# Kernel tuning notes

Hardware: AMD Instinct MI355X
Metric: run time of the kernel (lower is better)

The kernel has to match this reference:

```python
import jax, jax.numpy as jnp
import numpy as np

T, B, D = 2048, 8, 1024
TINY = float(np.finfo(np.float32).tiny)


def _uniform(k, shape, fan_in):
    b = 1.0 / np.sqrt(fan_in)
    return jax.random.uniform(k, shape, jnp.float32, -b, b)


def setup_inputs() -> dict:
    key = jax.random.key(0)
    ks = jax.random.split(key, 12)
    data = jax.random.normal(ks[0], (T, B, D), jnp.float32)
    return {
        "data": data,
        "qkv_w": _uniform(ks[1], (3 * D, D), D),
        "qkv_b": _uniform(ks[2], (3 * D,), D),
        "pos_bias": jax.random.normal(ks[3], (T, T), jnp.float32) * 0.02,
        "out_w": _uniform(ks[4], (D, D), D),
        "out_b": _uniform(ks[5], (D,), D),
        "fc1_w": _uniform(ks[6], (2 * D, D), D),
        "fc1_b": _uniform(ks[7], (2 * D,), D),
        "fc2_w": _uniform(ks[8], (D, D), D),
        "fc2_b": _uniform(ks[9], (D,), D),
    }


def _layer_norm(x):
    m = jnp.mean(x, axis=-1, keepdims=True)
    v = jnp.mean((x - m) ** 2, axis=-1, keepdims=True)
    return (x - m) / jnp.sqrt(v + TINY)


def _mish(x):
    return x * jnp.tanh(jax.nn.softplus(x))


def reference(data, qkv_w, qkv_b, pos_bias, out_w, out_b, fc1_w, fc1_b, fc2_w, fc2_b):
    # --- AFT branch --- data: [T, B, D]
    h = _layer_norm(data)
    qkv = h @ qkv_w.T + qkv_b                       # [T, B, 3D]
    q, k, v = jnp.split(qkv, 3, axis=-1)
    w = jnp.exp(pos_bias)                           # [T, T]
    ek = jnp.exp(k)                                 # [T, B, D]
    num = jnp.einsum('ij,jbd->ibd', w, ek * v)      # [T, B, D]
    den = jnp.einsum('ij,jbd->ibd', w, ek)
    aft = (jax.nn.sigmoid(q) * (num / den)) @ out_w.T + out_b
    # --- SwiGLU FFN branch ---
    h2 = _layer_norm(data)
    x12 = h2 @ fc1_w.T + fc1_b                      # [T, B, 2D]
    x1, gate = jnp.split(x12, 2, axis=-1)
    ffn = (x1 * _mish(gate)) @ fc2_w.T + fc2_b
    # --- parallel residual sum ---
    return data + aft + ffn
```

## Files before the change

kernel.cpp:

```cpp
#include <hip/hip_runtime.h>
#include <hip/hip_bf16.h>
#include <cmath>
#include <cstdint>

using bf16 = __hip_bfloat16;
typedef __attribute__((ext_vector_type(8))) short short8;
typedef __attribute__((ext_vector_type(4))) float f32x4;
typedef __attribute__((ext_vector_type(4))) unsigned short ushort4v;

#define T_DIM 2048
#define B_DIM 8
#define D_DIM 1024
#define MROWS (T_DIM*B_DIM)
#define N8 (B_DIM*D_DIM)

__device__ __forceinline__ float b2f(bf16 x) { return __bfloat162float(x); }
__device__ __forceinline__ bf16  f2b(float x) { return __float2bfloat16(x); }
__device__ __forceinline__ float us2f(unsigned short u) {
    union { unsigned int i; float f; } x; x.i = ((unsigned int)u) << 16; return x.f;
}
__device__ __forceinline__ unsigned short f2us(float f) {
    bf16 b = __float2bfloat16(f);
    return *(unsigned short*)&b;
}

__device__ __forceinline__ void gload_lds16(const bf16* g, bf16* l) {
    __builtin_amdgcn_global_load_lds(
        (const __attribute__((address_space(1))) unsigned int*)g,
        (__attribute__((address_space(3))) unsigned int*)l,
        16, 0, 0);
}

__global__ __launch_bounds__(256) void ln_kernel(const float* __restrict__ x,
                                                 bf16* __restrict__ h) {
    const int row = blockIdx.x;
    const int tid = threadIdx.x;
    const float4 v = ((const float4*)(x + (size_t)row * D_DIM))[tid];
    float s1 = v.x + v.y + v.z + v.w;
    float s2 = v.x*v.x + v.y*v.y + v.z*v.z + v.w*v.w;
    #pragma unroll
    for (int off = 32; off > 0; off >>= 1) {
        s1 += __shfl_down(s1, off);
        s2 += __shfl_down(s2, off);
    }
    __shared__ float red[8];
    const int lane = tid & 63, wv = tid >> 6;
    if (lane == 0) { red[wv*2] = s1; red[wv*2+1] = s2; }
    __syncthreads();
    s1 = red[0] + red[2] + red[4] + red[6];
    s2 = red[1] + red[3] + red[5] + red[7];
    const float mean = s1 * (1.0f / D_DIM);
    const float var  = s2 * (1.0f / D_DIM) - mean * mean;
    const float rstd = rsqrtf(var + 1.1754943508222875e-38f);
    bf16* hr = h + (size_t)row * D_DIM + tid * 4;
    hr[0] = f2b((v.x - mean) * rstd);
    hr[1] = f2b((v.y - mean) * rstd);
    hr[2] = f2b((v.z - mean) * rstd);
    hr[3] = f2b((v.w - mean) * rstd);
}

__global__ __launch_bounds__(256) void expw_kernel(const float* __restrict__ p,
                                                   bf16* __restrict__ w, int n4) {
    const int i = blockIdx.x * 256 + threadIdx.x;
    if (i < n4) {
        const float4 v = ((const float4*)p)[i];
        bf16* o = w + (size_t)i * 4;
        o[0] = f2b(expf(v.x)); o[1] = f2b(expf(v.y));
        o[2] = f2b(expf(v.z)); o[3] = f2b(expf(v.w));
    }
}

__global__ __launch_bounds__(256) void cvt_kernel(const float* __restrict__ p,
                                                  bf16* __restrict__ w, int n4) {
    const int i = blockIdx.x * 256 + threadIdx.x;
    if (i < n4) {
        const float4 v = ((const float4*)p)[i];
        bf16* o = w + (size_t)i * 4;
        o[0] = f2b(v.x); o[1] = f2b(v.y); o[2] = f2b(v.z); o[3] = f2b(v.w);
    }
}

__global__ __launch_bounds__(256) void transpose_ekv(
        const unsigned short* __restrict__ ek, const unsigned short* __restrict__ vv,
        unsigned short* __restrict__ EKt, unsigned short* __restrict__ EKVt) {
    __shared__ unsigned short le[64][68];
    __shared__ unsigned short lv[64][68];
    const int t0 = blockIdx.y * 64;
    const int n0 = blockIdx.x * 64;
    const int tid = threadIdx.x;
    const int r = tid >> 4;
    const int c = tid & 15;
    #pragma unroll
    for (int rr = 0; rr < 4; rr++) {
        const int row = rr * 16 + r;
        const size_t gi = (size_t)(t0 + row) * N8 + n0 + c * 4;
        const ushort4v e = *(const ushort4v*)(ek + gi);
        const ushort4v v = *(const ushort4v*)(vv + gi);
        *(ushort4v*)&le[row][c * 4] = e;
        *(ushort4v*)&lv[row][c * 4] = v;
    }
    __syncthreads();
    #pragma unroll
    for (int rr = 0; rr < 4; rr++) {
        const int nrow = rr * 16 + r;
        ushort4v eo, evo;
        #pragma unroll
        for (int j = 0; j < 4; j++) {
            const int tl = c * 4 + j;
            const unsigned short e = le[tl][nrow];
            const unsigned short v = lv[tl][nrow];
            eo[j]  = e;
            evo[j] = f2us(us2f(e) * us2f(v));
        }
        const size_t go = (size_t)(n0 + nrow) * T_DIM + t0 + c * 4;
        *(ushort4v*)(EKt + go)  = eo;
        *(ushort4v*)(EKVt + go) = evo;
    }
}

__global__ __launch_bounds__(256) void attn_combine(
        const unsigned short* __restrict__ C, const unsigned short* __restrict__ sq,
        unsigned short* __restrict__ Y) {
    const size_t i8 = (size_t)blockIdx.x * 256 + threadIdx.x;
    const size_t j0 = i8 * 8;
    const int t = (int)(j0 >> 13);
    const int u = (int)(j0 & 8191);
    const size_t cbase = (size_t)t * 16384 + u;
    const short8 den = *(const short8*)(C + cbase);
    const short8 num = *(const short8*)(C + cbase + 8192);
    const short8 s   = *(const short8*)(sq + j0);
    short8 y;
    #pragma unroll
    for (int j = 0; j < 8; j++) {
        const float n = us2f((unsigned short)num[j]);
        const float d = us2f((unsigned short)den[j]);
        const float sv = us2f((unsigned short)s[j]);
        y[j] = (short)f2us(sv * (n / d));
    }
    *(short8*)(Y + j0) = y;
}

__global__ __launch_bounds__(256) void glu_combine(
        const unsigned short* __restrict__ x12, unsigned short* __restrict__ ffin) {
    const size_t i8 = (size_t)blockIdx.x * 256 + threadIdx.x;
    const size_t j0 = i8 * 8;
    const int row = (int)(j0 >> 10);
    const int d = (int)(j0 & 1023);
    const size_t base = (size_t)row * 2048 + d;
    const short8 x1v = *(const short8*)(x12 + base);
    const short8 gv  = *(const short8*)(x12 + base + 1024);
    short8 o;
    #pragma unroll
    for (int j = 0; j < 8; j++) {
        const float x1 = us2f((unsigned short)x1v[j]);
        const float g  = us2f((unsigned short)gv[j]);
        const float sp = (g > 20.f) ? g : log1pf(expf(g));
        o[j] = (short)f2us(x1 * (g * tanhf(sp)));
    }
    *(short8*)(ffin + j0) = o;
}

enum { EPI_QKV = 0, EPI_BIAS_F32 = 1, EPI_FC2SUM = 2, EPI_STORE_BF16 = 3, EPI_BIAS_BF16 = 4 };

template <int M, int N, int K, int EPI>
__global__ __launch_bounds__(256, 1)
void gemm_bt(const bf16* __restrict__ A, const bf16* __restrict__ Bt,
             const float* __restrict__ bias,
             void* __restrict__ o0, void* __restrict__ o1, void* __restrict__ o2,
             const float* __restrict__ e1, const float* __restrict__ e2) {
    constexpr int BK = 32;
    __shared__ bf16 As[128 * BK];
    __shared__ bf16 Bs[128 * BK];
    const int tid = threadIdx.x;
    const int lane = tid & 63;
    const int wv = tid >> 6;
    const int wm = wv >> 1, wn = wv & 1;
    const int m0 = blockIdx.y * 128, n0 = blockIdx.x * 128;

    const int sr = tid >> 2;
    const int sc = (tid & 3) * 8;
    const bf16* gA = A  + (size_t)(m0 + sr) * K + sc;
    const bf16* gB = Bt + (size_t)(n0 + sr) * K + sc;
    bf16* lA0 = As + tid * 8;
    bf16* lA1 = As + 2048 + tid * 8;
    bf16* lB0 = Bs + tid * 8;
    bf16* lB1 = Bs + 2048 + tid * 8;
    const size_t gstep = (size_t)64 * K;

    f32x4 acc[4][4];
    #pragma unroll
    for (int i = 0; i < 4; i++)
        #pragma unroll
        for (int j = 0; j < 4; j++) acc[i][j] = (f32x4){0.f, 0.f, 0.f, 0.f};

    const int lr = lane & 15;
    const int lk = (lane >> 4) * 8;

    for (int kt = 0; kt < K; kt += BK) {
        __syncthreads();
        gload_lds16(gA + kt, lA0);
        gload_lds16(gA + kt + gstep, lA1);
        gload_lds16(gB + kt, lB0);
        gload_lds16(gB + kt + gstep, lB1);
        asm volatile("s_waitcnt vmcnt(0)");
        __syncthreads();
        short8 a[4], b[4];
        #pragma unroll
        for (int i = 0; i < 4; i++)
            a[i] = *(const short8*)&As[(wm * 64 + i * 16 + lr) * BK + lk];
        #pragma unroll
        for (int i = 0; i < 4; i++)
            b[i] = *(const short8*)&Bs[(wn * 64 + i * 16 + lr) * BK + lk];
        #pragma unroll
        for (int i = 0; i < 4; i++)
            #pragma unroll
            for (int j = 0; j < 4; j++)
                acc[i][j] = __builtin_amdgcn_mfma_f32_16x16x32_bf16(a[i], b[j], acc[i][j], 0, 0, 0);
    }

    const int rbase = (lane >> 4) * 4;
    #pragma unroll
    for (int i = 0; i < 4; i++) {
        #pragma unroll
        for (int j = 0; j < 4; j++) {
            const int col = n0 + wn * 64 + j * 16 + lr;
            float bv = 0.f;
            if constexpr (EPI != EPI_STORE_BF16) bv = bias[col];
            #pragma unroll
            for (int r = 0; r < 4; r++) {
                const int row = m0 + wm * 64 + i * 16 + rbase + r;
                const float c = acc[i][j][r] + bv;
                if constexpr (EPI == EPI_QKV) {
                    const int seg = col >> 10;
                    const int nn = col & 1023;
                    const size_t idx = (size_t)row * 1024 + nn;
                    if (seg == 0)      ((bf16*)o0)[idx] = f2b(1.f / (1.f + expf(-c)));
                    else if (seg == 1) ((bf16*)o1)[idx] = f2b(expf(c));
                    else               ((bf16*)o2)[idx] = f2b(c);
                } else if constexpr (EPI == EPI_BIAS_F32) {
                    ((float*)o0)[(size_t)row * N + col] = c;
                } else if constexpr (EPI == EPI_STORE_BF16 || EPI == EPI_BIAS_BF16) {
                    ((bf16*)o0)[(size_t)row * N + col] = f2b(c);
                } else {
                    const size_t idx = (size_t)row * N + col;
                    ((float*)o0)[idx] = c + e1[idx] + e2[idx];
                }
            }
        }
    }
}

extern "C" void kernel_launch(void* const* d_in, const int* in_sizes, int n_in,
                              void* d_out, int out_size, void* d_ws, size_t ws_size,
                              hipStream_t stream) {
    const float* data  = (const float*)d_in[0];
    const float* qkv_w = (const float*)d_in[1];
    const float* qkv_b = (const float*)d_in[2];
    const float* pos_b = (const float*)d_in[3];
    const float* out_w = (const float*)d_in[4];
    const float* out_b = (const float*)d_in[5];
    const float* fc1_w = (const float*)d_in[6];
    const float* fc1_b = (const float*)d_in[7];
    const float* fc2_w = (const float*)d_in[8];
    const float* fc2_b = (const float*)d_in[9];
    float* out = (float*)d_out;

    char* ws = (char*)d_ws;
    const size_t MB = 1024ull * 1024ull;
    bf16* h    = (bf16*)(ws);
    bf16* Wb   = (bf16*)(ws + 32*MB);
    bf16* sq   = (bf16*)(ws + 40*MB);
    char* slotA = ws + 72*MB;
    char* slotB = ws + 136*MB;
    bf16* qkvw_b = (bf16*)(ws + 200*MB);
    bf16* outw_b = qkvw_b + (size_t)3072 * 1024;
    bf16* fc1w_b = outw_b + (size_t)1024 * 1024;
    bf16* fc2w_b = fc1w_b + (size_t)2048 * 1024;

    bf16* ek   = (bf16*)slotA;
    bf16* vv   = (bf16*)(slotA + 32*MB);
    bf16* EKt  = (bf16*)slotB;
    bf16* EKVt = (bf16*)(slotB + 32*MB);
    bf16* Ccat = (bf16*)slotA;
    bf16* Y    = (bf16*)slotB;
    bf16* x12  = (bf16*)slotA;
    bf16* ffin = (bf16*)(slotB + 32*MB);

    ln_kernel<<<MROWS, 256, 0, stream>>>(data, h);
    expw_kernel<<<4096, 256, 0, stream>>>(pos_b, Wb, T_DIM * T_DIM / 4);
    cvt_kernel<<<3072, 256, 0, stream>>>(qkv_w, qkvw_b, 3072 * 1024 / 4);
    cvt_kernel<<<1024, 256, 0, stream>>>(out_w, outw_b, 1024 * 1024 / 4);
    cvt_kernel<<<2048, 256, 0, stream>>>(fc1_w, fc1w_b, 2048 * 1024 / 4);
    cvt_kernel<<<1024, 256, 0, stream>>>(fc2_w, fc2w_b, 1024 * 1024 / 4);

    gemm_bt<MROWS, 3072, 1024, EPI_QKV><<<dim3(24, 128), 256, 0, stream>>>(
        h, qkvw_b, qkv_b, sq, ek, vv, nullptr, nullptr);

    transpose_ekv<<<dim3(128, 32), 256, 0, stream>>>(
        (const unsigned short*)ek, (const unsigned short*)vv,
        (unsigned short*)EKt, (unsigned short*)EKVt);

    gemm_bt<T_DIM, 2 * N8, T_DIM, EPI_STORE_BF16><<<dim3(128, 16), 256, 0, stream>>>(
        Wb, EKt, nullptr, Ccat, nullptr, nullptr, nullptr, nullptr);

    attn_combine<<<8192, 256, 0, stream>>>(
        (const unsigned short*)Ccat, (const unsigned short*)sq, (unsigned short*)Y);

    gemm_bt<MROWS, 1024, 1024, EPI_BIAS_F32><<<dim3(8, 128), 256, 0, stream>>>(
        Y, outw_b, out_b, out, nullptr, nullptr, nullptr, nullptr);

    gemm_bt<MROWS, 2048, 1024, EPI_BIAS_BF16><<<dim3(16, 128), 256, 0, stream>>>(
        h, fc1w_b, fc1_b, x12, nullptr, nullptr, nullptr, nullptr);

    glu_combine<<<8192, 256, 0, stream>>>(
        (const unsigned short*)x12, (unsigned short*)ffin);

    gemm_bt<MROWS, 1024, 1024, EPI_FC2SUM><<<dim3(8, 128), 256, 0, stream>>>(
        ffin, fc2w_b, fc2_b, out, nullptr, nullptr, data, out);
}
```

Measured before the change: 801.5 us.

## Replace GEMM with 256x256 double-buffered 8-wave pipelined kernel

Replaces the simple 128x128, BK=32 single-buffered GEMM with a 256x256 tile kernel using 8 waves, BK=64, and 128KB of LDS double buffering. Global-to-LDS loads for the next K tile are interleaved with MFMA quads, separated by barriers and s_setprio. The kernel adds an XOR-swizzled LDS layout to avoid bank conflicts and remaps workgroups for L2 locality. The goal is to hide memory latency and raise MFMA utilization. The cost is more register pressure and a complex schedule whose vmcnt and barrier ordering must be exactly right.

```diff
diff --git a/kernel.cpp b/kernel.cpp
--- a/kernel.cpp
+++ b/kernel.cpp
@@ -24,7 +24,7 @@
     return *(unsigned short*)&b;
 }
 
-__device__ __forceinline__ void gload_lds16(const bf16* g, bf16* l) {
+__device__ __forceinline__ void gload_lds16(const bf16* g, char* l) {
     __builtin_amdgcn_global_load_lds(
         (const __attribute__((address_space(1))) unsigned int*)g,
         (__attribute__((address_space(3))) unsigned int*)l,
@@ -162,78 +162,136 @@
 
 enum { EPI_QKV = 0, EPI_BIAS_F32 = 1, EPI_FC2SUM = 2, EPI_STORE_BF16 = 3, EPI_BIAS_BF16 = 4 };
 
+#define BAR() __builtin_amdgcn_s_barrier()
+
+#define RD_A(ABASE, MOFF)                                                     \
+    _Pragma("unroll")                                                         \
+    for (int m = 0; m < 4; m++) {                                             \
+        a[m][0] = *(const short8*)(lds + (ABASE) + (MOFF + m) * 2048 + ck0);  \
+        a[m][1] = *(const short8*)(lds + (ABASE) + (MOFF + m) * 2048 + ck1);  \
+    }
+
+#define RD_B(BBASE, NOFF, BREG)                                               \
+    _Pragma("unroll")                                                         \
+    for (int n = 0; n < 2; n++) {                                             \
+        BREG[n][0] = *(const short8*)(lds + (BBASE) + (NOFF + n) * 2048 + ck0);\
+        BREG[n][1] = *(const short8*)(lds + (BBASE) + (NOFF + n) * 2048 + ck1);\
+    }
+
+#define MFMA_QUAD(MB, NB, BREG)                                               \
+    __builtin_amdgcn_s_setprio(1);                                            \
+    _Pragma("unroll")                                                         \
+    for (int m = 0; m < 4; m++) {                                             \
+        _Pragma("unroll")                                                     \
+        for (int n = 0; n < 2; n++) {                                         \
+            acc[MB + m][NB + n] = __builtin_amdgcn_mfma_f32_16x16x32_bf16(    \
+                a[m][0], BREG[n][0], acc[MB + m][NB + n], 0, 0, 0);           \
+            acc[MB + m][NB + n] = __builtin_amdgcn_mfma_f32_16x16x32_bf16(    \
+                a[m][1], BREG[n][1], acc[MB + m][NB + n], 0, 0, 0);           \
+        }                                                                     \
+    }                                                                         \
+    __builtin_amdgcn_s_setprio(0);
+
 template <int M, int N, int K, int EPI>
-__global__ __launch_bounds__(256, 1)
-void gemm_bt(const bf16* __restrict__ A, const bf16* __restrict__ Bt,
-             const float* __restrict__ bias,
-             void* __restrict__ o0, void* __restrict__ o1, void* __restrict__ o2,
-             const float* __restrict__ e1, const float* __restrict__ e2) {
-    constexpr int BK = 32;
-    __shared__ bf16 As[128 * BK];
-    __shared__ bf16 Bs[128 * BK];
+__global__ __launch_bounds__(512, 2)
+void gemm8(const bf16* __restrict__ A, const bf16* __restrict__ Bt,
+           const float* __restrict__ bias,
+           void* __restrict__ o0, void* __restrict__ o1, void* __restrict__ o2,
+           const float* __restrict__ e1, const float* __restrict__ e2) {
+    constexpr int NK = K / 64;
+    constexpr int NIT = NK / 2;
+    constexpr int KMASK = NK - 1;
+    __shared__ char lds[131072];
     const int tid = threadIdx.x;
     const int lane = tid & 63;
-    const int wv = tid >> 6;
-    const int wm = wv >> 1, wn = wv & 1;
-    const int m0 = blockIdx.y * 128, n0 = blockIdx.x * 128;
-
-    const int sr = tid >> 2;
-    const int sc = (tid & 3) * 8;
-    const bf16* gA = A  + (size_t)(m0 + sr) * K + sc;
-    const bf16* gB = Bt + (size_t)(n0 + sr) * K + sc;
-    bf16* lA0 = As + tid * 8;
-    bf16* lA1 = As + 2048 + tid * 8;
-    bf16* lB0 = Bs + tid * 8;
-    bf16* lB1 = Bs + 2048 + tid * 8;
-    const size_t gstep = (size_t)64 * K;
-
-    f32x4 acc[4][4];
-    #pragma unroll
-    for (int i = 0; i < 4; i++)
+    const int wid = tid >> 6;
+    const int wr = wid >> 2, wc = wid & 3;
+    const int lr = lane & 15;
+
+    const int nwg = gridDim.x * gridDim.y;
+    int lin = blockIdx.y * gridDim.x + blockIdx.x;
+    lin = (lin & 7) * (nwg >> 3) + (lin >> 3);
+    const int bx = lin % gridDim.x, by = lin / gridDim.x;
+    const int m0 = by * 256, n0 = bx * 256;
+
+    const int srow = tid >> 3;
+    const int scol = ((tid & 7) * 8) ^ (((tid >> 5) & 1) << 4);
+    const int sdst = tid * 16;
+
+    const int cx  = ((lane >> 2) & 1) << 5;
+    const int ck0 = (((lane >> 4) * 16)) ^ cx;
+    const int ck1 = (64 + ((lane >> 4) * 16)) ^ cx;
+    const int abase0 = wr * 16384 + lr * 128;
+    const int abase1 = 65536 + abase0;
+    const int bbase0 = 32768 + (wc >> 1) * 16384 + ((wc & 1) * 64 + lr) * 128;
+    const int bbase1 = 65536 + bbase0;
+
+    auto STAGE = [&](const bf16* P, int r0, int kt, int ldsoff) {
+        gload_lds16(P + (size_t)(r0 + srow) * K + kt + scol, lds + ldsoff + sdst);
+        gload_lds16(P + (size_t)(r0 + 64 + srow) * K + kt + scol,
+                    lds + ldsoff + 8192 + sdst);
+    };
+
+    f32x4 acc[8][4] = {};
+    short8 a[4][2], blo[2][2], bhi[2][2];
+
+    STAGE(A,  m0,       0, 0);
+    STAGE(A,  m0 + 128, 0, 16384);
+    STAGE(Bt, n0,       0, 32768);
+    STAGE(Bt, n0 + 128, 0, 49152);
+    STAGE(Bt, n0,      64, 65536 + 32768);
+    STAGE(A,  m0,      64, 65536);
+    asm volatile("s_waitcnt vmcnt(4)");
+    BAR();
+
+    for (int i = 0; i < NIT; ++i) {
+        const int t1k = ((2 * i + 1) & KMASK) * 64;
+        const int t2k = ((2 * i + 2) & KMASK) * 64;
+        const int t3k = ((2 * i + 3) & KMASK) * 64;
+        RD_A(abase0, 0); RD_B(bbase0, 0, blo);
+        STAGE(Bt, n0 + 128, t1k, 65536 + 49152);
+        BAR(); MFMA_QUAD(0, 0, blo); BAR();
+        RD_B(bbase0, 2, bhi);
+        STAGE(A, m0 + 128, t1k, 65536 + 16384);
+        BAR(); MFMA_QUAD(0, 2, bhi); BAR();
+        RD_A(abase0, 4);
+        STAGE(Bt, n0, t2k, 32768);
+        BAR(); MFMA_QUAD(4, 2, bhi); BAR();
+        STAGE(A, m0, t2k, 0);
+        asm volatile("s_waitcnt vmcnt(4)");
+        BAR(); MFMA_QUAD(4, 0, blo); BAR();
+        RD_A(abase1, 0); RD_B(bbase1, 0, blo);
+        STAGE(A, m0 + 128, t2k, 16384);
+        BAR(); MFMA_QUAD(0, 0, blo); BAR();
+        RD_B(bbase1, 2, bhi);
+        STAGE(Bt, n0 + 128, t2k, 49152);
+        BAR(); MFMA_QUAD(0, 2, bhi); BAR();
+        RD_A(abase1, 4);
+        STAGE(Bt, n0, t3k, 65536 + 32768);
+        BAR(); MFMA_QUAD(4, 2, bhi); BAR();
+        STAGE(A, m0, t3k, 65536);
+        asm volatile("s_waitcnt vmcnt(4)");
+        BAR(); MFMA_QUAD(4, 0, blo); BAR();
+    }
+    asm volatile("s_waitcnt vmcnt(0)");
+
+    const int rb = (lane >> 4) * 4;
+    #pragma unroll
+    for (int mm = 0; mm < 8; mm++) {
         #pragma unroll
-        for (int j = 0; j < 4; j++) acc[i][j] = (f32x4){0.f, 0.f, 0.f, 0.f};
-
-    const int lr = lane & 15;
-    const int lk = (lane >> 4) * 8;
-
-    for (int kt = 0; kt < K; kt += BK) {
-        __syncthreads();
-        gload_lds16(gA + kt, lA0);
-        gload_lds16(gA + kt + gstep, lA1);
-        gload_lds16(gB + kt, lB0);
-        gload_lds16(gB + kt + gstep, lB1);
-        asm volatile("s_waitcnt vmcnt(0)");
-        __syncthreads();
-        short8 a[4], b[4];
-        #pragma unroll
-        for (int i = 0; i < 4; i++)
-            a[i] = *(const short8*)&As[(wm * 64 + i * 16 + lr) * BK + lk];
-        #pragma unroll
-        for (int i = 0; i < 4; i++)
-            b[i] = *(const short8*)&Bs[(wn * 64 + i * 16 + lr) * BK + lk];
-        #pragma unroll
-        for (int i = 0; i < 4; i++)
-            #pragma unroll
-            for (int j = 0; j < 4; j++)
-                acc[i][j] = __builtin_amdgcn_mfma_f32_16x16x32_bf16(a[i], b[j], acc[i][j], 0, 0, 0);
-    }
-
-    const int rbase = (lane >> 4) * 4;
-    #pragma unroll
-    for (int i = 0; i < 4; i++) {
-        #pragma unroll
-        for (int j = 0; j < 4; j++) {
-            const int col = n0 + wn * 64 + j * 16 + lr;
+        for (int nn = 0; nn < 4; nn++) {
+            const int col = n0 + wc * 64 + nn * 16 + lr;
             float bv = 0.f;
             if constexpr (EPI != EPI_STORE_BF16) bv = bias[col];
+            const int row0 = m0 + wr * 128 + mm * 16 + rb;
             #pragma unroll
             for (int r = 0; r < 4; r++) {
-                const int row = m0 + wm * 64 + i * 16 + rbase + r;
-                const float c = acc[i][j][r] + bv;
+                const int row = row0 + r;
+                const float c = acc[mm][nn][r] + bv;
                 if constexpr (EPI == EPI_QKV) {
                     const int seg = col >> 10;
-                    const int nn = col & 1023;
-                    const size_t idx = (size_t)row * 1024 + nn;
+                    const int nc = col & 1023;
+                    const size_t idx = (size_t)row * 1024 + nc;
                     if (seg == 0)      ((bf16*)o0)[idx] = f2b(1.f / (1.f + expf(-c)));
                     else if (seg == 1) ((bf16*)o1)[idx] = f2b(expf(c));
                     else               ((bf16*)o2)[idx] = f2b(c);
@@ -293,28 +351,28 @@
     cvt_kernel<<<2048, 256, 0, stream>>>(fc1_w, fc1w_b, 2048 * 1024 / 4);
     cvt_kernel<<<1024, 256, 0, stream>>>(fc2_w, fc2w_b, 1024 * 1024 / 4);
 
-    gemm_bt<MROWS, 3072, 1024, EPI_QKV><<<dim3(24, 128), 256, 0, stream>>>(
+    gemm8<MROWS, 3072, 1024, EPI_QKV><<<dim3(12, 64), 512, 0, stream>>>(
         h, qkvw_b, qkv_b, sq, ek, vv, nullptr, nullptr);
 
     transpose_ekv<<<dim3(128, 32), 256, 0, stream>>>(
         (const unsigned short*)ek, (const unsigned short*)vv,
         (unsigned short*)EKt, (unsigned short*)EKVt);
 
-    gemm_bt<T_DIM, 2 * N8, T_DIM, EPI_STORE_BF16><<<dim3(128, 16), 256, 0, stream>>>(
+    gemm8<T_DIM, 2 * N8, T_DIM, EPI_STORE_BF16><<<dim3(64, 8), 512, 0, stream>>>(
         Wb, EKt, nullptr, Ccat, nullptr, nullptr, nullptr, nullptr);
 
     attn_combine<<<8192, 256, 0, stream>>>(
         (const unsigned short*)Ccat, (const unsigned short*)sq, (unsigned short*)Y);
 
-    gemm_bt<MROWS, 1024, 1024, EPI_BIAS_F32><<<dim3(8, 128), 256, 0, stream>>>(
+    gemm8<MROWS, 1024, 1024, EPI_BIAS_F32><<<dim3(4, 64), 512, 0, stream>>>(
         Y, outw_b, out_b, out, nullptr, nullptr, nullptr, nullptr);
 
-    gemm_bt<MROWS, 2048, 1024, EPI_BIAS_BF16><<<dim3(16, 128), 256, 0, stream>>>(
+    gemm8<MROWS, 2048, 1024, EPI_BIAS_BF16><<<dim3(8, 64), 512, 0, stream>>>(
         h, fc1w_b, fc1_b, x12, nullptr, nullptr, nullptr, nullptr);
 
     glu_combine<<<8192, 256, 0, stream>>>(
         (const unsigned short*)x12, (unsigned short*)ffin);
 
-    gemm_bt<MROWS, 1024, 1024, EPI_FC2SUM><<<dim3(8, 128), 256, 0, stream>>>(
+    gemm8<MROWS, 1024, 1024, EPI_FC2SUM><<<dim3(4, 64), 512, 0, stream>>>(
         ffin, fc2w_b, fc2_b, out, nullptr, nullptr, data, out);
 }
```

Measured after the change: 728.5 us. -9.1%, faster.
